# Kernel optimization log

Measured on AMD Instinct MI355X. Metric: run time of the kernel, lower is better.

## Reference

```python
import jax, jax.numpy as jnp
import numpy as np

N_SEND = 12288   # 12 * 32^2
N_REC = 49152    # 12 * 64^2
E = 196608       # 4 * N_REC (knn with k=4)
D = 256
EIN, EOUT = 4, 256
LIN_IN, LIN_OUT = 512, 256
B = 2


def setup_inputs() -> dict:
    key = jax.random.key(0)
    ks = jax.random.split(key, 12)
    s = 0.05
    x = jax.random.normal(ks[0], (B, N_SEND, D), jnp.float32)
    edge_attr = jax.random.normal(ks[1], (E, EIN), jnp.float32)
    idx_send = jax.random.randint(ks[2], (E,), 0, N_SEND, dtype=jnp.int32)
    idx_rec = jnp.sort(jax.random.randint(ks[3], (E,), 0, N_REC, dtype=jnp.int32))
    return {
        "x": x,
        "edge_attr": edge_attr,
        "idx_send": idx_send,
        "idx_rec": idx_rec,
        "We1": jax.random.normal(ks[4], (EIN, EOUT), jnp.float32) * s,
        "be1": jnp.zeros((EOUT,), jnp.float32),
        "We2": jax.random.normal(ks[5], (EOUT, EOUT), jnp.float32) * s,
        "be2": jnp.zeros((EOUT,), jnp.float32),
        "Wl1": jax.random.normal(ks[6], (LIN_IN, LIN_OUT), jnp.float32) * s,
        "bl1": jnp.zeros((LIN_OUT,), jnp.float32),
        "Wl2": jax.random.normal(ks[7], (LIN_OUT, LIN_OUT), jnp.float32) * s,
        "bl2": jnp.zeros((LIN_OUT,), jnp.float32),
    }


def reference(x, edge_attr, idx_send, idx_rec, We1, be1, We2, be2, Wl1, bl1, Wl2, bl2):
    # edge embedder MLP: Linear -> GELU -> Linear   [E, EOUT]
    ef = jax.nn.gelu(edge_attr @ We1 + be1) @ We2 + be2
    # gather sender node features by edge           [B, E, D]
    v_s = x[:, idx_send, :]
    # concat gathered features with (batch-broadcast) edge embeddings [B, E, D+EOUT]
    ef_b = jnp.broadcast_to(ef[None], (v_s.shape[0],) + ef.shape)
    v_s_prime = jnp.concatenate([v_s, ef_b], axis=-1)
    # scatter_sum over receiver index along edge dim -> [B, N_REC, LIN_IN]
    agg = jax.vmap(lambda m: jax.ops.segment_sum(m, idx_rec, num_segments=N_REC))(v_s_prime)
    # final FeedForward: Linear -> GELU -> Linear
    return jax.nn.gelu(agg @ Wl1 + bl1) @ Wl2 + bl2
```

## Files before the change

### kernel.cpp

```cpp
#include <hip/hip_runtime.h>
#include <hip/hip_bf16.h>

#define N_SEND 12288
#define N_REC  49152
#define NEDGE  196608
#define ECAP   512

typedef __attribute__((ext_vector_type(8)))  short short8;
typedef __attribute__((ext_vector_type(4)))  short shortx4;
typedef __attribute__((ext_vector_type(4)))  float floatx4;
typedef __attribute__((ext_vector_type(16))) float floatx16;
typedef __attribute__((ext_vector_type(4)))  unsigned int uintx4;

__device__ inline short f2bs(float f) {
    __hip_bfloat16 h = __float2bfloat16(f);
    return *reinterpret_cast<short*>(&h);
}
__device__ inline float gelu_tanh(float x) {
    const float k0 = 0.7978845608028654f;
    float u = k0 * (x + 0.044715f * x * x * x);
    float e = __expf(2.0f * u);
    float t = 1.0f - 2.0f / (e + 1.0f);
    return 0.5f * x * (1.0f + t);
}

__global__ void prep_kernel(const float* __restrict__ We2, const float* __restrict__ be2,
                            const float* __restrict__ Wl1, const float* __restrict__ Wl2,
                            short* __restrict__ BT1, short* __restrict__ WT2,
                            float* __restrict__ cvec) {
    int i = blockIdx.x;
    int n = threadIdx.x;
    if (i < 256) {
        float acc = 0.f;
        for (int j = 0; j < 256; ++j)
            acc += We2[i * 256 + j] * Wl1[(256 + j) * 256 + n];
        BT1[n * 512 + i]       = f2bs(Wl1[i * 256 + n]);
        BT1[n * 512 + 256 + i] = f2bs(acc);
        WT2[n * 256 + i]       = f2bs(Wl2[i * 256 + n]);
    } else {
        float acc = 0.f;
        for (int j = 0; j < 256; ++j)
            acc += be2[j] * Wl1[(256 + j) * 256 + n];
        cvec[n] = acc;
    }
}

__global__ void xcast_kernel(const float* __restrict__ X, short* __restrict__ Xb) {
    int i = (blockIdx.x * 256 + threadIdx.x) * 8;
    floatx4 v0 = *(const floatx4*)(X + i);
    floatx4 v1 = *(const floatx4*)(X + i + 4);
    short8 p;
#pragma unroll
    for (int j = 0; j < 4; ++j) { p[j] = f2bs(v0[j]); p[j + 4] = f2bs(v1[j]); }
    *(short8*)(Xb + i) = p;
}

__global__ void bounds_kernel(const int* __restrict__ idx_rec, int* __restrict__ bnd) {
    int r = blockIdx.x * 256 + threadIdx.x;
    if (r > N_REC) return;
    int lo = 0, hi = NEDGE;
    while (lo < hi) { int mid = (lo + hi) >> 1; if (idx_rec[mid] < r) lo = mid + 1; else hi = mid; }
    bnd[r] = lo;
}

__global__ __launch_bounds__(512, 2)
void fused(const int* __restrict__ idx_send, const int* __restrict__ bnd,
           const float* __restrict__ EA, const float* __restrict__ We1,
           const float* __restrict__ be1, const short* __restrict__ Xb,
           const short* __restrict__ BT1, const short* __restrict__ WT2,
           const float* __restrict__ cvec, const float* __restrict__ bl1,
           const float* __restrict__ bl2, float* __restrict__ OUT) {
    __shared__ short XT[32 * 128 * 8];
    __shared__ short HT[32 * 64 * 8];
    __shared__ int   sb[65];
    __shared__ int   s_idx[ECAP];
    __shared__ float s_ea[ECAP * 4];

    int t = threadIdx.x;
    int r0 = blockIdx.x * 64;
    if (t < 65) sb[t] = bnd[r0 + t];
    __syncthreads();
    int e0 = sb[0], eN = sb[64];

    {
        int cg = t & 31;
        int b  = (t >> 5) & 1;
        int rh = t >> 6;
        int c8 = cg * 8;
        int hc = c8 + 4 * b;

        floatx4 w0 = *(const floatx4*)(We1 + hc);
        floatx4 w1 = *(const floatx4*)(We1 + 256 + hc);
        floatx4 w2 = *(const floatx4*)(We1 + 512 + hc);
        floatx4 w3 = *(const floatx4*)(We1 + 768 + hc);
        floatx4 bb = *(const floatx4*)(be1 + hc);
        const short* xb_t = Xb + (size_t)b * N_SEND * 256 + c8;

        float xacc[8][8];
        float hacc[8][4];
#pragma unroll
        for (int r = 0; r < 8; ++r) {
#pragma unroll
            for (int c = 0; c < 8; ++c) xacc[r][c] = 0.f;
#pragma unroll
            for (int c = 0; c < 4; ++c) hacc[r][c] = 0.f;
        }

        for (int base = e0; base < eN; base += ECAP) {
            int cnt = min(ECAP, eN - base);
            __syncthreads();
            for (int i = t; i < cnt; i += 512) {
                s_idx[i] = idx_send[base + i];
                *(floatx4*)(s_ea + 4 * i) = *(const floatx4*)(EA + (size_t)(base + i) * 4);
            }
            __syncthreads();
#pragma unroll
            for (int r = 0; r < 8; ++r) {
                int rl = rh * 8 + r;
                int es = max(sb[rl], base);
                int ee = min(sb[rl + 1], base + cnt);
                for (int e = es; e < ee; ++e) {
                    int li = e - base;
                    int s = s_idx[li];
                    uintx4 xv = *(const uintx4*)(xb_t + (size_t)s * 256);
                    floatx4 a = *(const floatx4*)(s_ea + 4 * li);
#pragma unroll
                    for (int dw = 0; dw < 4; ++dw) {
                        xacc[r][2 * dw]     += __builtin_bit_cast(float, xv[dw] << 16);
                        xacc[r][2 * dw + 1] += __builtin_bit_cast(float, xv[dw] & 0xffff0000u);
                    }
#pragma unroll
                    for (int j = 0; j < 4; ++j) {
                        float u = a[0] * w0[j] + a[1] * w1[j] + a[2] * w2[j] + a[3] * w3[j] + bb[j];
                        hacc[r][j] += gelu_tanh(u);
                    }
                }
            }
        }
#pragma unroll
        for (int r = 0; r < 8; ++r) {
            int rl = rh * 8 + r;
            int row = b * 64 + rl;
            short8 xp;
#pragma unroll
            for (int c = 0; c < 8; ++c) xp[c] = f2bs(xacc[r][c]);
            *(short8*)(XT + (cg * 128 + row) * 8) = xp;
            shortx4 hp;
#pragma unroll
            for (int c = 0; c < 4; ++c) hp[c] = f2bs(hacc[r][c]);
            *(shortx4*)(HT + (cg * 64 + rl) * 8 + 4 * b) = hp;
        }
    }
    __syncthreads();

    int w = t >> 6, lane = t & 63;
    int m = lane & 31, q = lane >> 5;
    int wcol = w * 32;
    floatx16 acc[4];
#pragma unroll
    for (int i = 0; i < 4; ++i)
#pragma unroll
        for (int j = 0; j < 16; ++j) acc[i][j] = 0.f;

    const short* Bp1 = BT1 + (size_t)(wcol + m) * 512 + q * 8;
    short8 bfA[4], bfB[4];
#pragma unroll
    for (int kk = 0; kk < 4; ++kk) bfA[kk] = *(const short8*)(Bp1 + kk * 16);

#pragma unroll
    for (int ci = 0; ci < 8; ++ci) {
        int kc = ci * 64;
        const short8* bc = (ci & 1) ? bfB : bfA;
        short8*       bn = (ci & 1) ? bfA : bfB;
        if (ci < 7) {
#pragma unroll
            for (int kk = 0; kk < 4; ++kk)
                bn[kk] = *(const short8*)(Bp1 + kc + 64 + kk * 16);
        }
#pragma unroll
        for (int kk = 0; kk < 4; ++kk) {
            int f = (kc >> 3) + 2 * kk + q;
#pragma unroll
            for (int rt = 0; rt < 4; ++rt) {
                int row = rt * 32 + m;
                const short* ap = (ci < 4)
                    ? (XT + (f * 128 + row) * 8)
                    : (HT + ((f - 32) * 64 + (row & 63)) * 8);
                short8 a = *(const short8*)ap;
                acc[rt] = __builtin_amdgcn_mfma_f32_32x32x16_bf16(bc[kk], a, acc[rt], 0, 0, 0);
            }
        }
    }
    __syncthreads();

#pragma unroll
    for (int rt = 0; rt < 4; ++rt) {
        int row = rt * 32 + m;
        int rl = row & 63;
        float cntv = (float)(sb[rl + 1] - sb[rl]);
#pragma unroll
        for (int qd = 0; qd < 4; ++qd) {
            int c0 = wcol + qd * 8 + q * 4;
            floatx4 cv  = *(const floatx4*)(cvec + c0);
            floatx4 b1v = *(const floatx4*)(bl1 + c0);
            shortx4 pk;
#pragma unroll
            for (int j = 0; j < 4; ++j)
                pk[j] = f2bs(gelu_tanh(acc[rt][qd * 4 + j] + cntv * cv[j] + b1v[j]));
            *(shortx4*)(XT + ((w * 4 + qd) * 128 + row) * 8 + q * 4) = pk;
        }
#pragma unroll
        for (int j = 0; j < 16; ++j) acc[rt][j] = 0.f;
    }
    __syncthreads();

    const short* Bp2 = WT2 + (size_t)(wcol + m) * 256 + q * 8;
#pragma unroll
    for (int kk = 0; kk < 4; ++kk) bfA[kk] = *(const short8*)(Bp2 + kk * 16);

#pragma unroll
    for (int ci = 0; ci < 4; ++ci) {
        int kc = ci * 64;
        const short8* bc = (ci & 1) ? bfB : bfA;
        short8*       bn = (ci & 1) ? bfA : bfB;
        if (ci < 3) {
#pragma unroll
            for (int kk = 0; kk < 4; ++kk)
                bn[kk] = *(const short8*)(Bp2 + kc + 64 + kk * 16);
        }
#pragma unroll
        for (int kk = 0; kk < 4; ++kk) {
            int f2 = (kc >> 3) + 2 * kk + q;
#pragma unroll
            for (int rt = 0; rt < 4; ++rt) {
                short8 a = *(const short8*)(XT + (f2 * 128 + rt * 32 + m) * 8);
                acc[rt] = __builtin_amdgcn_mfma_f32_32x32x16_bf16(bc[kk], a, acc[rt], 0, 0, 0);
            }
        }
    }

#pragma unroll
    for (int rt = 0; rt < 4; ++rt) {
        int row = rt * 32 + m;
        int batch = row >> 6;
        int rl = row & 63;
        size_t obase = ((size_t)batch * N_REC + r0 + rl) * 256;
#pragma unroll
        for (int qd = 0; qd < 4; ++qd) {
            int c0 = wcol + qd * 8 + q * 4;
            floatx4 bv = *(const floatx4*)(bl2 + c0);
            floatx4 o;
#pragma unroll
            for (int j = 0; j < 4; ++j)
                o[j] = acc[rt][qd * 4 + j] + bv[j];
            *(floatx4*)(OUT + obase + c0) = o;
        }
    }
}

extern "C" void kernel_launch(void* const* d_in, const int* in_sizes, int n_in,
                              void* d_out, int out_size, void* d_ws, size_t ws_size,
                              hipStream_t stream) {
    const float* x        = (const float*)d_in[0];
    const float* ea       = (const float*)d_in[1];
    const int*   idx_send = (const int*)d_in[2];
    const int*   idx_rec  = (const int*)d_in[3];
    const float* We1      = (const float*)d_in[4];
    const float* be1      = (const float*)d_in[5];
    const float* We2      = (const float*)d_in[6];
    const float* be2      = (const float*)d_in[7];
    const float* Wl1      = (const float*)d_in[8];
    const float* bl1      = (const float*)d_in[9];
    const float* Wl2      = (const float*)d_in[10];
    const float* bl2      = (const float*)d_in[11];
    float* out = (float*)d_out;
    char*  ws  = (char*)d_ws;

    short* BT1  = (short*)(ws + 0);
    short* WT2  = (short*)(ws + 262144);
    float* cvec = (float*)(ws + 393216);
    int*   bnd  = (int*)  (ws + 397312);
    short* Xb   = (short*)(ws + 1048576);

    prep_kernel<<<257, 256, 0, stream>>>(We2, be2, Wl1, Wl2, BT1, WT2, cvec);
    xcast_kernel<<<(2 * N_SEND * 256) / (256 * 8), 256, 0, stream>>>(x, Xb);
    bounds_kernel<<<(N_REC + 1 + 255) / 256, 256, 0, stream>>>(idx_rec, bnd);
    fused<<<N_REC / 64, 512, 0, stream>>>(idx_send, bnd, ea, We1, be1, Xb,
                                          BT1, WT2, cvec, bl1, bl2, out);
}
```

Measured before the change: 286.6 us.

## Split fused kernel into high-occupancy aggregate pass and separate MFMA GEMM pass

Splits the fused gather-aggregate-plus-MLP kernel in two. An aggregate kernel handles 16 receivers per block at higher occupancy (launch bounds 6) and writes bf16 aggregates to workspace in an MFMA-ready tiled layout. A GEMM kernel then loads those tiles straight into LDS with global_load_lds and runs the two MFMA layers. The aim is to hide the latency of the irregular gather with more resident waves, since the old kernel's large register and LDS footprint limited occupancy. The cost is an extra global round trip for the intermediate (about 75 MB write plus read) and one more launch.

New measurement: 297.4 us. +3.7%, slower.

```diff
diff --git a/kernel.cpp b/kernel.cpp
--- a/kernel.cpp
+++ b/kernel.cpp
@@ -4,7 +4,8 @@
 #define N_SEND 12288
 #define N_REC  49152
 #define NEDGE  196608
-#define ECAP   512
+#define AREC   16
+#define AECAP  256
 
 typedef __attribute__((ext_vector_type(8)))  short short8;
 typedef __attribute__((ext_vector_type(4)))  short shortx4;
@@ -22,6 +23,12 @@
     float e = __expf(2.0f * u);
     float t = 1.0f - 2.0f / (e + 1.0f);
     return 0.5f * x * (1.0f + t);
+}
+
+__device__ inline void gload_lds16(const short* g, short* l) {
+    __builtin_amdgcn_global_load_lds(
+        (const __attribute__((address_space(1))) unsigned int*)g,
+        (__attribute__((address_space(3))) unsigned int*)l, 16, 0, 0);
 }
 
 __global__ void prep_kernel(const float* __restrict__ We2, const float* __restrict__ be2,
@@ -63,92 +70,128 @@
     bnd[r] = lo;
 }
 
-__global__ __launch_bounds__(512, 2)
-void fused(const int* __restrict__ idx_send, const int* __restrict__ bnd,
-           const float* __restrict__ EA, const float* __restrict__ We1,
-           const float* __restrict__ be1, const short* __restrict__ Xb,
-           const short* __restrict__ BT1, const short* __restrict__ WT2,
-           const float* __restrict__ cvec, const float* __restrict__ bl1,
-           const float* __restrict__ bl2, float* __restrict__ OUT) {
-    __shared__ short XT[32 * 128 * 8];
-    __shared__ short HT[32 * 64 * 8];
-    __shared__ int   sb[65];
-    __shared__ int   s_idx[ECAP];
-    __shared__ float s_ea[ECAP * 4];
+__global__ __launch_bounds__(512, 6)
+void aggregate(const int* __restrict__ idx_send, const int* __restrict__ bnd,
+               const float* __restrict__ EA, const float* __restrict__ We1,
+               const float* __restrict__ be1, const short* __restrict__ Xb,
+               short* __restrict__ AGX, short* __restrict__ AGH) {
+    __shared__ __attribute__((aligned(16))) short XTs[32 * 32 * 8];
+    __shared__ __attribute__((aligned(16))) short HTs[32 * 16 * 8];
+    __shared__ int   sb[AREC + 1];
+    __shared__ int   s_idx[AECAP];
+    __shared__ __attribute__((aligned(16))) float s_ea[AECAP * 4];
 
     int t = threadIdx.x;
-    int r0 = blockIdx.x * 64;
-    if (t < 65) sb[t] = bnd[r0 + t];
-    __syncthreads();
-    int e0 = sb[0], eN = sb[64];
-
-    {
-        int cg = t & 31;
-        int b  = (t >> 5) & 1;
-        int rh = t >> 6;
-        int c8 = cg * 8;
-        int hc = c8 + 4 * b;
-
-        floatx4 w0 = *(const floatx4*)(We1 + hc);
-        floatx4 w1 = *(const floatx4*)(We1 + 256 + hc);
-        floatx4 w2 = *(const floatx4*)(We1 + 512 + hc);
-        floatx4 w3 = *(const floatx4*)(We1 + 768 + hc);
-        floatx4 bb = *(const floatx4*)(be1 + hc);
-        const short* xb_t = Xb + (size_t)b * N_SEND * 256 + c8;
-
-        float xacc[8][8];
-        float hacc[8][4];
-#pragma unroll
-        for (int r = 0; r < 8; ++r) {
-#pragma unroll
-            for (int c = 0; c < 8; ++c) xacc[r][c] = 0.f;
-#pragma unroll
-            for (int c = 0; c < 4; ++c) hacc[r][c] = 0.f;
-        }
-
-        for (int base = e0; base < eN; base += ECAP) {
-            int cnt = min(ECAP, eN - base);
-            __syncthreads();
-            for (int i = t; i < cnt; i += 512) {
-                s_idx[i] = idx_send[base + i];
-                *(floatx4*)(s_ea + 4 * i) = *(const floatx4*)(EA + (size_t)(base + i) * 4);
-            }
-            __syncthreads();
-#pragma unroll
-            for (int r = 0; r < 8; ++r) {
-                int rl = rh * 8 + r;
-                int es = max(sb[rl], base);
-                int ee = min(sb[rl + 1], base + cnt);
-                for (int e = es; e < ee; ++e) {
-                    int li = e - base;
-                    int s = s_idx[li];
-                    uintx4 xv = *(const uintx4*)(xb_t + (size_t)s * 256);
-                    floatx4 a = *(const floatx4*)(s_ea + 4 * li);
-#pragma unroll
-                    for (int dw = 0; dw < 4; ++dw) {
-                        xacc[r][2 * dw]     += __builtin_bit_cast(float, xv[dw] << 16);
-                        xacc[r][2 * dw + 1] += __builtin_bit_cast(float, xv[dw] & 0xffff0000u);
-                    }
-#pragma unroll
-                    for (int j = 0; j < 4; ++j) {
-                        float u = a[0] * w0[j] + a[1] * w1[j] + a[2] * w2[j] + a[3] * w3[j] + bb[j];
-                        hacc[r][j] += gelu_tanh(u);
-                    }
+    int r0 = blockIdx.x * AREC;
+    if (t <= AREC) sb[t] = bnd[r0 + t];
+    __syncthreads();
+    int e0 = sb[0], eN = sb[AREC];
+
+    int cg = t & 31;
+    int b  = (t >> 5) & 1;
+    int rh = t >> 6;
+    int c8 = cg * 8;
+    int hc = c8 + 4 * b;
+
+    floatx4 w0 = *(const floatx4*)(We1 + hc);
+    floatx4 w1 = *(const floatx4*)(We1 + 256 + hc);
+    floatx4 w2 = *(const floatx4*)(We1 + 512 + hc);
+    floatx4 w3 = *(const floatx4*)(We1 + 768 + hc);
+    floatx4 bb = *(const floatx4*)(be1 + hc);
+    const short* xb_t = Xb + (size_t)b * N_SEND * 256 + c8;
+
+    float xacc[2][8];
+    float hacc[2][4];
+#pragma unroll
+    for (int r = 0; r < 2; ++r) {
+#pragma unroll
+        for (int c = 0; c < 8; ++c) xacc[r][c] = 0.f;
+#pragma unroll
+        for (int c = 0; c < 4; ++c) hacc[r][c] = 0.f;
+    }
+
+    for (int base = e0; base < eN; base += AECAP) {
+        int cnt = min(AECAP, eN - base);
+        __syncthreads();
+        for (int i = t; i < cnt; i += 512) {
+            s_idx[i] = idx_send[base + i];
+            *(floatx4*)(s_ea + 4 * i) = *(const floatx4*)(EA + (size_t)(base + i) * 4);
+        }
+        __syncthreads();
+#pragma unroll
+        for (int r = 0; r < 2; ++r) {
+            int rl = rh * 2 + r;
+            int es = max(sb[rl], base);
+            int ee = min(sb[rl + 1], base + cnt);
+            for (int e = es; e < ee; ++e) {
+                int li = e - base;
+                int s = s_idx[li];
+                uintx4 xv = *(const uintx4*)(xb_t + (size_t)s * 256);
+                floatx4 a = *(const floatx4*)(s_ea + 4 * li);
+#pragma unroll
+                for (int dw = 0; dw < 4; ++dw) {
+                    xacc[r][2 * dw]     += __builtin_bit_cast(float, xv[dw] << 16);
+                    xacc[r][2 * dw + 1] += __builtin_bit_cast(float, xv[dw] & 0xffff0000u);
+                }
+#pragma unroll
+                for (int j = 0; j < 4; ++j) {
+                    float u = a[0] * w0[j] + a[1] * w1[j] + a[2] * w2[j] + a[3] * w3[j] + bb[j];
+                    hacc[r][j] += gelu_tanh(u);
                 }
             }
         }
-#pragma unroll
-        for (int r = 0; r < 8; ++r) {
-            int rl = rh * 8 + r;
-            int row = b * 64 + rl;
-            short8 xp;
-#pragma unroll
-            for (int c = 0; c < 8; ++c) xp[c] = f2bs(xacc[r][c]);
-            *(short8*)(XT + (cg * 128 + row) * 8) = xp;
-            shortx4 hp;
-#pragma unroll
-            for (int c = 0; c < 4; ++c) hp[c] = f2bs(hacc[r][c]);
-            *(shortx4*)(HT + (cg * 64 + rl) * 8 + 4 * b) = hp;
+    }
+#pragma unroll
+    for (int r = 0; r < 2; ++r) {
+        int rl = rh * 2 + r;
+        short8 xp;
+#pragma unroll
+        for (int c = 0; c < 8; ++c) xp[c] = f2bs(xacc[r][c]);
+        *(short8*)(XTs + (cg * 32 + b * 16 + rl) * 8) = xp;
+        shortx4 hp;
+#pragma unroll
+        for (int c = 0; c < 4; ++c) hp[c] = f2bs(hacc[r][c]);
+        *(shortx4*)(HTs + (cg * 16 + rl) * 8 + 4 * b) = hp;
+    }
+    __syncthreads();
+    {
+        const uintx4* xs = (const uintx4*)XTs;
+        uintx4* xd = (uintx4*)(AGX + (size_t)blockIdx.x * (32 * 32 * 8));
+        xd[t]       = xs[t];
+        xd[t + 512] = xs[t + 512];
+        const uintx4* hs = (const uintx4*)HTs;
+        uintx4* hd = (uintx4*)(AGH + (size_t)blockIdx.x * (32 * 16 * 8));
+        hd[t] = hs[t];
+    }
+}
+
+__global__ __launch_bounds__(512, 2)
+void gemm(const int* __restrict__ bnd, const short* __restrict__ AGX,
+          const short* __restrict__ AGH, const short* __restrict__ BT1,
+          const short* __restrict__ WT2, const float* __restrict__ cvec,
+          const float* __restrict__ bl1, const float* __restrict__ bl2,
+          float* __restrict__ OUT) {
+    __shared__ __attribute__((aligned(16))) short XT[4 * 32 * 32 * 8];
+    __shared__ __attribute__((aligned(16))) short HT[4 * 32 * 16 * 8];
+    __shared__ int sb[65];
+
+    int t = threadIdx.x;
+    int blk = blockIdx.x;
+    int r0 = blk * 64;
+    if (t < 65) sb[t] = bnd[r0 + t];
+
+    {
+        const short* sx = AGX + (size_t)blk * (4 * 32 * 32 * 8);
+        const short* sh = AGH + (size_t)blk * (4 * 32 * 16 * 8);
+#pragma unroll
+        for (int k = 0; k < 8; ++k) {
+            int c = t + k * 512;
+            gload_lds16(sx + c * 8, XT + c * 8);
+        }
+#pragma unroll
+        for (int k = 0; k < 4; ++k) {
+            int c = t + k * 512;
+            gload_lds16(sh + c * 8, HT + c * 8);
         }
     }
     __syncthreads();
@@ -182,10 +225,9 @@
             int f = (kc >> 3) + 2 * kk + q;
 #pragma unroll
             for (int rt = 0; rt < 4; ++rt) {
-                int row = rt * 32 + m;
                 const short* ap = (ci < 4)
-                    ? (XT + (f * 128 + row) * 8)
-                    : (HT + ((f - 32) * 64 + (row & 63)) * 8);
+                    ? (XT + rt * 8192 + f * 256 + m * 8)
+                    : (HT + rt * 4096 + (f - 32) * 128 + (m & 15) * 8);
                 short8 a = *(const short8*)ap;
                 acc[rt] = __builtin_amdgcn_mfma_f32_32x32x16_bf16(bc[kk], a, acc[rt], 0, 0, 0);
             }
@@ -196,7 +238,7 @@
 #pragma unroll
     for (int rt = 0; rt < 4; ++rt) {
         int row = rt * 32 + m;
-        int rl = row & 63;
+        int rl = rt * 16 + (m & 15);
         float cntv = (float)(sb[rl + 1] - sb[rl]);
 #pragma unroll
         for (int qd = 0; qd < 4; ++qd) {
@@ -241,9 +283,8 @@
 
 #pragma unroll
     for (int rt = 0; rt < 4; ++rt) {
-        int row = rt * 32 + m;
-        int batch = row >> 6;
-        int rl = row & 63;
+        int batch = (m >> 4) & 1;
+        int rl = rt * 16 + (m & 15);
         size_t obase = ((size_t)batch * N_REC + r0 + rl) * 256;
 #pragma unroll
         for (int qd = 0; qd < 4; ++qd) {
@@ -281,10 +322,12 @@
     float* cvec = (float*)(ws + 393216);
     int*   bnd  = (int*)  (ws + 397312);
     short* Xb   = (short*)(ws + 1048576);
+    short* AGX  = (short*)(ws + 13631488);
+    short* AGH  = (short*)(ws + 63963136);
 
     prep_kernel<<<257, 256, 0, stream>>>(We2, be2, Wl1, Wl2, BT1, WT2, cvec);
     xcast_kernel<<<(2 * N_SEND * 256) / (256 * 8), 256, 0, stream>>>(x, Xb);
     bounds_kernel<<<(N_REC + 1 + 255) / 256, 256, 0, stream>>>(idx_rec, bnd);
-    fused<<<N_REC / 64, 512, 0, stream>>>(idx_send, bnd, ea, We1, be1, Xb,
-                                          BT1, WT2, cvec, bl1, bl2, out);
-}
+    aggregate<<<N_REC / AREC, 512, 0, stream>>>(idx_send, bnd, ea, We1, be1, Xb, AGX, AGH);
+    gemm<<<N_REC / 64, 512, 0, stream>>>(bnd, AGX, AGH, BT1, WT2, cvec, bl1, bl2, out);
+}
```

## Halve receiver tile to 32 rows, raise occupancy, swizzle LDS tiles

Applied to the files above, without the earlier changes.

The fused kernel now processes 32 receivers per block instead of 64. It launches twice as many blocks and requests 6 blocks per CU instead of 2 through launch bounds. Edge indices and attributes are read directly from global memory per receiver instead of being staged in shared memory, and the LDS tile layouts get an XOR swizzle to reduce bank conflicts. The aim is more waves in flight to hide gather latency. In exchange, B-operand weight loads are no longer double-buffered and each weight matrix is reloaded by twice as many blocks.

New measurement: 310.4 us. 1.08x slower.

```diff
diff --git a/kernel.cpp b/kernel.cpp
--- a/kernel.cpp
+++ b/kernel.cpp
@@ -4,7 +4,6 @@
 #define N_SEND 12288
 #define N_REC  49152
 #define NEDGE  196608
-#define ECAP   512
 
 typedef __attribute__((ext_vector_type(8)))  short short8;
 typedef __attribute__((ext_vector_type(4)))  short shortx4;
@@ -63,24 +62,24 @@
     bnd[r] = lo;
 }
 
-__global__ __launch_bounds__(512, 2)
-void fused(const int* __restrict__ idx_send, const int* __restrict__ bnd,
-           const float* __restrict__ EA, const float* __restrict__ We1,
-           const float* __restrict__ be1, const short* __restrict__ Xb,
-           const short* __restrict__ BT1, const short* __restrict__ WT2,
-           const float* __restrict__ cvec, const float* __restrict__ bl1,
-           const float* __restrict__ bl2, float* __restrict__ OUT) {
-    __shared__ short XT[32 * 128 * 8];
-    __shared__ short HT[32 * 64 * 8];
-    __shared__ int   sb[65];
-    __shared__ int   s_idx[ECAP];
-    __shared__ float s_ea[ECAP * 4];
+#define XTU(f, row) ((((f) * 64) + ((row) ^ ((f) & 7))) * 8)
+#define HTU(f, rl)  ((((f) * 32) + ((rl) ^ ((f) & 7))) * 8)
+
+__global__ __launch_bounds__(512, 6)
+void fused32(const int* __restrict__ idx_send, const int* __restrict__ bnd,
+             const float* __restrict__ EA, const float* __restrict__ We1,
+             const float* __restrict__ be1, const short* __restrict__ Xb,
+             const short* __restrict__ BT1, const short* __restrict__ WT2,
+             const float* __restrict__ cvec, const float* __restrict__ bl1,
+             const float* __restrict__ bl2, float* __restrict__ OUT) {
+    __shared__ __attribute__((aligned(16))) short XT[32 * 64 * 8];
+    __shared__ __attribute__((aligned(16))) short HT[32 * 32 * 8];
+    __shared__ int sb[33];
 
     int t = threadIdx.x;
-    int r0 = blockIdx.x * 64;
-    if (t < 65) sb[t] = bnd[r0 + t];
-    __syncthreads();
-    int e0 = sb[0], eN = sb[64];
+    int r0 = blockIdx.x * 32;
+    if (t <= 32) sb[t] = bnd[r0 + t];
+    __syncthreads();
 
     {
         int cg = t & 31;
@@ -96,59 +95,42 @@
         floatx4 bb = *(const floatx4*)(be1 + hc);
         const short* xb_t = Xb + (size_t)b * N_SEND * 256 + c8;
 
-        float xacc[8][8];
-        float hacc[8][4];
-#pragma unroll
-        for (int r = 0; r < 8; ++r) {
-#pragma unroll
-            for (int c = 0; c < 8; ++c) xacc[r][c] = 0.f;
-#pragma unroll
-            for (int c = 0; c < 4; ++c) hacc[r][c] = 0.f;
-        }
-
-        for (int base = e0; base < eN; base += ECAP) {
-            int cnt = min(ECAP, eN - base);
-            __syncthreads();
-            for (int i = t; i < cnt; i += 512) {
-                s_idx[i] = idx_send[base + i];
-                *(floatx4*)(s_ea + 4 * i) = *(const floatx4*)(EA + (size_t)(base + i) * 4);
-            }
-            __syncthreads();
-#pragma unroll
-            for (int r = 0; r < 8; ++r) {
-                int rl = rh * 8 + r;
-                int es = max(sb[rl], base);
-                int ee = min(sb[rl + 1], base + cnt);
-                for (int e = es; e < ee; ++e) {
-                    int li = e - base;
-                    int s = s_idx[li];
-                    uintx4 xv = *(const uintx4*)(xb_t + (size_t)s * 256);
-                    floatx4 a = *(const floatx4*)(s_ea + 4 * li);
-#pragma unroll
-                    for (int dw = 0; dw < 4; ++dw) {
-                        xacc[r][2 * dw]     += __builtin_bit_cast(float, xv[dw] << 16);
-                        xacc[r][2 * dw + 1] += __builtin_bit_cast(float, xv[dw] & 0xffff0000u);
-                    }
-#pragma unroll
-                    for (int j = 0; j < 4; ++j) {
-                        float u = a[0] * w0[j] + a[1] * w1[j] + a[2] * w2[j] + a[3] * w3[j] + bb[j];
-                        hacc[r][j] += gelu_tanh(u);
-                    }
+#pragma unroll
+        for (int r = 0; r < 4; ++r) {
+            int rl = rh * 4 + r;
+            int es = __builtin_amdgcn_readfirstlane(sb[rl]);
+            int ee = __builtin_amdgcn_readfirstlane(sb[rl + 1]);
+
+            float xacc[8];
+            float hacc[4];
+#pragma unroll
+            for (int c = 0; c < 8; ++c) xacc[c] = 0.f;
+#pragma unroll
+            for (int c = 0; c < 4; ++c) hacc[c] = 0.f;
+
+            for (int e = es; e < ee; ++e) {
+                int s = idx_send[e];
+                floatx4 a = *(const floatx4*)(EA + (size_t)e * 4);
+                uintx4 xv = *(const uintx4*)(xb_t + (size_t)s * 256);
+#pragma unroll
+                for (int dw = 0; dw < 4; ++dw) {
+                    xacc[2 * dw]     += __builtin_bit_cast(float, xv[dw] << 16);
+                    xacc[2 * dw + 1] += __builtin_bit_cast(float, xv[dw] & 0xffff0000u);
+                }
+#pragma unroll
+                for (int j = 0; j < 4; ++j) {
+                    float u = a[0] * w0[j] + a[1] * w1[j] + a[2] * w2[j] + a[3] * w3[j] + bb[j];
+                    hacc[j] += gelu_tanh(u);
                 }
             }
-        }
-#pragma unroll
-        for (int r = 0; r < 8; ++r) {
-            int rl = rh * 8 + r;
-            int row = b * 64 + rl;
             short8 xp;
 #pragma unroll
-            for (int c = 0; c < 8; ++c) xp[c] = f2bs(xacc[r][c]);
-            *(short8*)(XT + (cg * 128 + row) * 8) = xp;
+            for (int c = 0; c < 8; ++c) xp[c] = f2bs(xacc[c]);
+            *(short8*)(XT + XTU(cg, b * 32 + rl)) = xp;
             shortx4 hp;
 #pragma unroll
-            for (int c = 0; c < 4; ++c) hp[c] = f2bs(hacc[r][c]);
-            *(shortx4*)(HT + (cg * 64 + rl) * 8 + 4 * b) = hp;
+            for (int c = 0; c < 4; ++c) hp[c] = f2bs(hacc[c]);
+            *(shortx4*)(HT + HTU(cg, rl) + 4 * b) = hp;
         }
     }
     __syncthreads();
@@ -156,95 +138,74 @@
     int w = t >> 6, lane = t & 63;
     int m = lane & 31, q = lane >> 5;
     int wcol = w * 32;
-    floatx16 acc[4];
-#pragma unroll
-    for (int i = 0; i < 4; ++i)
-#pragma unroll
-        for (int j = 0; j < 16; ++j) acc[i][j] = 0.f;
+    floatx16 acc0, acc1;
+#pragma unroll
+    for (int j = 0; j < 16; ++j) { acc0[j] = 0.f; acc1[j] = 0.f; }
 
     const short* Bp1 = BT1 + (size_t)(wcol + m) * 512 + q * 8;
-    short8 bfA[4], bfB[4];
-#pragma unroll
-    for (int kk = 0; kk < 4; ++kk) bfA[kk] = *(const short8*)(Bp1 + kk * 16);
-
 #pragma unroll
     for (int ci = 0; ci < 8; ++ci) {
-        int kc = ci * 64;
-        const short8* bc = (ci & 1) ? bfB : bfA;
-        short8*       bn = (ci & 1) ? bfA : bfB;
-        if (ci < 7) {
-#pragma unroll
-            for (int kk = 0; kk < 4; ++kk)
-                bn[kk] = *(const short8*)(Bp1 + kc + 64 + kk * 16);
-        }
+        short8 bf[4];
+#pragma unroll
+        for (int kk = 0; kk < 4; ++kk) bf[kk] = *(const short8*)(Bp1 + ci * 64 + kk * 16);
 #pragma unroll
         for (int kk = 0; kk < 4; ++kk) {
-            int f = (kc >> 3) + 2 * kk + q;
-#pragma unroll
-            for (int rt = 0; rt < 4; ++rt) {
-                int row = rt * 32 + m;
-                const short* ap = (ci < 4)
-                    ? (XT + (f * 128 + row) * 8)
-                    : (HT + ((f - 32) * 64 + (row & 63)) * 8);
-                short8 a = *(const short8*)ap;
-                acc[rt] = __builtin_amdgcn_mfma_f32_32x32x16_bf16(bc[kk], a, acc[rt], 0, 0, 0);
+            int f = ci * 8 + 2 * kk + q;
+            short8 a0, a1;
+            if (ci < 4) {
+                a0 = *(const short8*)(XT + XTU(f, m));
+                a1 = *(const short8*)(XT + XTU(f, 32 + m));
+            } else {
+                a0 = *(const short8*)(HT + HTU(f - 32, m));
+                a1 = a0;
             }
-        }
-    }
-    __syncthreads();
-
-#pragma unroll
-    for (int rt = 0; rt < 4; ++rt) {
-        int row = rt * 32 + m;
-        int rl = row & 63;
-        float cntv = (float)(sb[rl + 1] - sb[rl]);
+            acc0 = __builtin_amdgcn_mfma_f32_32x32x16_bf16(bf[kk], a0, acc0, 0, 0, 0);
+            acc1 = __builtin_amdgcn_mfma_f32_32x32x16_bf16(bf[kk], a1, acc1, 0, 0, 0);
+        }
+    }
+    __syncthreads();
+
+    {
+        float cntv = (float)(sb[m + 1] - sb[m]);
 #pragma unroll
         for (int qd = 0; qd < 4; ++qd) {
             int c0 = wcol + qd * 8 + q * 4;
             floatx4 cv  = *(const floatx4*)(cvec + c0);
             floatx4 b1v = *(const floatx4*)(bl1 + c0);
-            shortx4 pk;
-#pragma unroll
-            for (int j = 0; j < 4; ++j)
-                pk[j] = f2bs(gelu_tanh(acc[rt][qd * 4 + j] + cntv * cv[j] + b1v[j]));
-            *(shortx4*)(XT + ((w * 4 + qd) * 128 + row) * 8 + q * 4) = pk;
-        }
-#pragma unroll
-        for (int j = 0; j < 16; ++j) acc[rt][j] = 0.f;
+            shortx4 p0, p1;
+#pragma unroll
+            for (int j = 0; j < 4; ++j) {
+                p0[j] = f2bs(gelu_tanh(acc0[qd * 4 + j] + cntv * cv[j] + b1v[j]));
+                p1[j] = f2bs(gelu_tanh(acc1[qd * 4 + j] + cntv * cv[j] + b1v[j]));
+            }
+            *(shortx4*)(XT + XTU(w * 4 + qd, m)      + q * 4) = p0;
+            *(shortx4*)(XT + XTU(w * 4 + qd, 32 + m) + q * 4) = p1;
+        }
+#pragma unroll
+        for (int j = 0; j < 16; ++j) { acc0[j] = 0.f; acc1[j] = 0.f; }
     }
     __syncthreads();
 
     const short* Bp2 = WT2 + (size_t)(wcol + m) * 256 + q * 8;
 #pragma unroll
-    for (int kk = 0; kk < 4; ++kk) bfA[kk] = *(const short8*)(Bp2 + kk * 16);
-
-#pragma unroll
     for (int ci = 0; ci < 4; ++ci) {
-        int kc = ci * 64;
-        const short8* bc = (ci & 1) ? bfB : bfA;
-        short8*       bn = (ci & 1) ? bfA : bfB;
-        if (ci < 3) {
-#pragma unroll
-            for (int kk = 0; kk < 4; ++kk)
-                bn[kk] = *(const short8*)(Bp2 + kc + 64 + kk * 16);
-        }
+        short8 bf[4];
+#pragma unroll
+        for (int kk = 0; kk < 4; ++kk) bf[kk] = *(const short8*)(Bp2 + ci * 64 + kk * 16);
 #pragma unroll
         for (int kk = 0; kk < 4; ++kk) {
-            int f2 = (kc >> 3) + 2 * kk + q;
-#pragma unroll
-            for (int rt = 0; rt < 4; ++rt) {
-                short8 a = *(const short8*)(XT + (f2 * 128 + rt * 32 + m) * 8);
-                acc[rt] = __builtin_amdgcn_mfma_f32_32x32x16_bf16(bc[kk], a, acc[rt], 0, 0, 0);
-            }
-        }
-    }
-
-#pragma unroll
-    for (int rt = 0; rt < 4; ++rt) {
-        int row = rt * 32 + m;
-        int batch = row >> 6;
-        int rl = row & 63;
-        size_t obase = ((size_t)batch * N_REC + r0 + rl) * 256;
+            int f2 = ci * 8 + 2 * kk + q;
+            short8 a0 = *(const short8*)(XT + XTU(f2, m));
+            short8 a1 = *(const short8*)(XT + XTU(f2, 32 + m));
+            acc0 = __builtin_amdgcn_mfma_f32_32x32x16_bf16(bf[kk], a0, acc0, 0, 0, 0);
+            acc1 = __builtin_amdgcn_mfma_f32_32x32x16_bf16(bf[kk], a1, acc1, 0, 0, 0);
+        }
+    }
+
+#pragma unroll
+    for (int rt = 0; rt < 2; ++rt) {
+        const floatx16& ac = rt ? acc1 : acc0;
+        size_t obase = ((size_t)rt * N_REC + r0 + m) * 256;
 #pragma unroll
         for (int qd = 0; qd < 4; ++qd) {
             int c0 = wcol + qd * 8 + q * 4;
@@ -252,7 +213,7 @@
             floatx4 o;
 #pragma unroll
             for (int j = 0; j < 4; ++j)
-                o[j] = acc[rt][qd * 4 + j] + bv[j];
+                o[j] = ac[qd * 4 + j] + bv[j];
             *(floatx4*)(OUT + obase + c0) = o;
         }
     }
@@ -285,6 +246,6 @@
     prep_kernel<<<257, 256, 0, stream>>>(We2, be2, Wl1, Wl2, BT1, WT2, cvec);
     xcast_kernel<<<(2 * N_SEND * 256) / (256 * 8), 256, 0, stream>>>(x, Xb);
     bounds_kernel<<<(N_REC + 1 + 255) / 256, 256, 0, stream>>>(idx_rec, bnd);
-    fused<<<N_REC / 64, 512, 0, stream>>>(idx_send, bnd, ea, We1, be1, Xb,
-                                          BT1, WT2, cvec, bl1, bl2, out);
-}
+    fused32<<<N_REC / 32, 512, 0, stream>>>(idx_send, bnd, ea, We1, be1, Xb,
+                                            BT1, WT2, cvec, bl1, bl2, out);
+}
```
